# Kernel tuning notes

Hardware: AMD Instinct MI355X
Metric: run time of the kernel (lower is better)

Reference implementation:

```python
import jax, jax.numpy as jnp
import numpy as np

NIN = 128
NOUT = 128


def setup_inputs() -> dict:
    key = jax.random.key(0)
    k_adj, k_node, k_wi, k_wj = jax.random.split(key, 4)
    B, N = 4, 256
    adj = jax.random.uniform(k_adj, (B, 1, N, N), dtype=jnp.float32)
    node = jax.random.normal(k_node, (B, NIN, N), dtype=jnp.float32)
    # 1x1 conv weights, stored as [nout, nin] (squeezed from [nout, nin, 1, 1])
    scale = 1.0 / np.sqrt(NIN)
    Wi = jax.random.normal(k_wi, (NOUT, NIN), dtype=jnp.float32) * scale
    Wj = jax.random.normal(k_wj, (NOUT, NIN), dtype=jnp.float32) * scale
    return {"adj": adj, "node": node, "Wi": Wi, "Wj": Wj}


def reference(adj, node, Wi, Wj):
    # adj: [B,1,N,N], node: [B,nin,N]
    N = adj.shape[-1]
    # broadcast node across rows and mask by adjacency: [B,nin,N,N]
    x = node[:, :, None, :] * adj
    # 1x1 convs == channel contractions
    yi = jnp.einsum('oc,bcij->boij', Wi, x)
    yj = jnp.einsum('oc,bcij->boij', Wj, x)
    I = jnp.eye(N, dtype=x.dtype)
    return I * yi + (1.0 - I) * yj
```

## Files before the change

kernel.cpp:

```cpp
#include <hip/hip_runtime.h>

#define NIN  128
#define NOUT 128
#define NN   256
#define BB   4

__global__ __launch_bounds__(256) void nodeconv_kernel(
    const float* __restrict__ adj,
    const float* __restrict__ node,
    const float* __restrict__ Wi,
    const float* __restrict__ Wj,
    float* __restrict__ out)
{
    __shared__ float si[NN];
    __shared__ float sj[NN];

    const int bo = blockIdx.x;
    const int b  = bo >> 7;
    const int o  = bo & (NOUT - 1);
    const int t  = threadIdx.x;

    {
        const float* np_ = node + (size_t)(b * NIN) * NN + t;
        const float* wi  = Wi + o * NIN;
        const float* wj  = Wj + o * NIN;
        float ai = 0.f, aj = 0.f;
        #pragma unroll 8
        for (int c = 0; c < NIN; ++c) {
            const float n = np_[(size_t)c * NN];
            ai += wi[c] * n;
            aj += wj[c] * n;
        }
        si[t] = ai;
        sj[t] = aj;
    }
    __syncthreads();

    const int j4   = t & 63;
    const int jb   = j4 << 2;
    const int rrow = t >> 6;

    const float4 vj = *(const float4*)&sj[jb];

    const float* adjb = adj + (size_t)b * (NN * NN);
    float*       outp = out + (size_t)bo * (NN * NN);

    #pragma unroll 4
    for (int r = 0; r < 64; ++r) {
        const int i = (r << 2) + rrow;
        const float s_ii = si[i];
        const float4 a = *(const float4*)&adjb[i * NN + jb];
        float4 v;
        v.x = (i == jb + 0) ? s_ii : vj.x;
        v.y = (i == jb + 1) ? s_ii : vj.y;
        v.z = (i == jb + 2) ? s_ii : vj.z;
        v.w = (i == jb + 3) ? s_ii : vj.w;
        float4 rs;
        rs.x = a.x * v.x;
        rs.y = a.y * v.y;
        rs.z = a.z * v.z;
        rs.w = a.w * v.w;
        *(float4*)&outp[i * NN + jb] = rs;
    }
}

extern "C" void kernel_launch(void* const* d_in, const int* in_sizes, int n_in,
                              void* d_out, int out_size, void* d_ws, size_t ws_size,
                              hipStream_t stream) {
    const float* adj  = (const float*)d_in[0];
    const float* node = (const float*)d_in[1];
    const float* Wi   = (const float*)d_in[2];
    const float* Wj   = (const float*)d_in[3];
    float* out = (float*)d_out;

    dim3 grid(BB * NOUT);
    dim3 block(256);
    nodeconv_kernel<<<grid, block, 0, stream>>>(adj, node, Wi, Wj, out);
}
```

Before: 184.8 us.

## Split projection into precompute kernel and widen streaming grid eightfold

Moves the per-(batch,output) channel projection into its own kernel that writes ui/uj to workspace. A second kernel then streams adj times the projected values over a grid eight times larger, each block handling 32 rows. The aim is better occupancy and more latency hiding for the bandwidth-bound output write, since the old grid had only 512 blocks. The cost is an extra launch and a small workspace round trip. A fused fallback is kept for when the workspace is too small.

```diff
diff --git a/kernel.cpp b/kernel.cpp
--- a/kernel.cpp
+++ b/kernel.cpp
@@ -5,21 +5,83 @@
 #define NN   256
 #define BB   4
 
-__global__ __launch_bounds__(256) void nodeconv_kernel(
-    const float* __restrict__ adj,
+__global__ __launch_bounds__(256) void precompute_u(
     const float* __restrict__ node,
     const float* __restrict__ Wi,
     const float* __restrict__ Wj,
-    float* __restrict__ out)
+    float* __restrict__ ui,
+    float* __restrict__ uj)
 {
-    __shared__ float si[NN];
-    __shared__ float sj[NN];
-
     const int bo = blockIdx.x;
     const int b  = bo >> 7;
     const int o  = bo & (NOUT - 1);
     const int t  = threadIdx.x;
 
+    const float* np_ = node + (size_t)b * NIN * NN + t;
+    const float* wi  = Wi + o * NIN;
+    const float* wj  = Wj + o * NIN;
+
+    float ai = 0.f, aj = 0.f;
+    #pragma unroll 16
+    for (int c = 0; c < NIN; ++c) {
+        const float n = np_[c * NN];
+        ai = fmaf(wi[c], n, ai);
+        aj = fmaf(wj[c], n, aj);
+    }
+    ui[bo * NN + t] = ai;
+    uj[bo * NN + t] = aj;
+}
+
+__global__ __launch_bounds__(256) void stream_out(
+    const float* __restrict__ adj,
+    const float* __restrict__ ui,
+    const float* __restrict__ uj,
+    float* __restrict__ out)
+{
+    const int blk = blockIdx.x;
+    const int bo  = blk >> 3;
+    const int rc  = blk & 7;
+    const int b   = bo >> 7;
+    const int t   = threadIdx.x;
+    const int jb  = (t & 63) << 2;
+    const int rr  = t >> 6;
+
+    const float4 vj   = *(const float4*)&uj[bo * NN + jb];
+    const float* uip  = ui + bo * NN;
+    const float* adjb = adj + (size_t)b * (NN * NN);
+    float*       outp = out + (size_t)bo * (NN * NN);
+
+    const int i0 = (rc << 5) + rr;
+    #pragma unroll
+    for (int r = 0; r < 8; ++r) {
+        const int i = i0 + (r << 2);
+        const float s_ii = uip[i];
+        const float4 a = *(const float4*)&adjb[i * NN + jb];
+        float4 v;
+        v.x = (i == jb + 0) ? s_ii : vj.x;
+        v.y = (i == jb + 1) ? s_ii : vj.y;
+        v.z = (i == jb + 2) ? s_ii : vj.z;
+        v.w = (i == jb + 3) ? s_ii : vj.w;
+        float4 rs;
+        rs.x = a.x * v.x;
+        rs.y = a.y * v.y;
+        rs.z = a.z * v.z;
+        rs.w = a.w * v.w;
+        *(float4*)&outp[i * NN + jb] = rs;
+    }
+}
+
+__global__ __launch_bounds__(256) void nodeconv_fused(
+    const float* __restrict__ adj, const float* __restrict__ node,
+    const float* __restrict__ Wi, const float* __restrict__ Wj,
+    float* __restrict__ out)
+{
+    __shared__ float si[NN];
+    __shared__ float sj[NN];
+    const int bo = blockIdx.x;
+    const int b  = bo >> 7;
+    const int o  = bo & (NOUT - 1);
+    const int t  = threadIdx.x;
     {
         const float* np_ = node + (size_t)(b * NIN) * NN + t;
         const float* wi  = Wi + o * NIN;
@@ -35,16 +97,11 @@
         sj[t] = aj;
     }
     __syncthreads();
-
-    const int j4   = t & 63;
-    const int jb   = j4 << 2;
+    const int jb   = (t & 63) << 2;
     const int rrow = t >> 6;
-
     const float4 vj = *(const float4*)&sj[jb];
-
     const float* adjb = adj + (size_t)b * (NN * NN);
     float*       outp = out + (size_t)bo * (NN * NN);
-
     #pragma unroll 4
     for (int r = 0; r < 64; ++r) {
         const int i = (r << 2) + rrow;
@@ -56,10 +113,7 @@
         v.z = (i == jb + 2) ? s_ii : vj.z;
         v.w = (i == jb + 3) ? s_ii : vj.w;
         float4 rs;
-        rs.x = a.x * v.x;
-        rs.y = a.y * v.y;
-        rs.z = a.z * v.z;
-        rs.w = a.w * v.w;
+        rs.x = a.x * v.x; rs.y = a.y * v.y; rs.z = a.z * v.z; rs.w = a.w * v.w;
         *(float4*)&outp[i * NN + jb] = rs;
     }
 }
@@ -73,7 +127,15 @@
     const float* Wj   = (const float*)d_in[3];
     float* out = (float*)d_out;
 
-    dim3 grid(BB * NOUT);
-    dim3 block(256);
-    nodeconv_kernel<<<grid, block, 0, stream>>>(adj, node, Wi, Wj, out);
+    const size_t u_elems = (size_t)BB * NOUT * NN;
+    const size_t need    = 2 * u_elems * sizeof(float);
+
+    if (ws_size >= need) {
+        float* ui = (float*)d_ws;
+        float* uj = ui + u_elems;
+        precompute_u<<<dim3(BB * NOUT), dim3(256), 0, stream>>>(node, Wi, Wj, ui, uj);
+        stream_out<<<dim3(BB * NOUT * 8), dim3(256), 0, stream>>>(adj, ui, uj, out);
+    } else {
+        nodeconv_fused<<<dim3(BB * NOUT), dim3(256), 0, stream>>>(adj, node, Wi, Wj, out);
+    }
 }
```

Result: faster. 148.4 us (-19.7%).

## Use 1024-thread blocks with split-channel projection and nontemporal output stores

Applied to the files above, without the earlier changes.

Each block grows from 256 to 1024 threads. The per-node projection is split across four thread groups (two weight matrices times two halves of the channel dimension) and reduced through shared memory, which shortens the serial 128-step dot product. Each thread then writes 16 contiguous rows instead of 64 strided ones, using nontemporal stores for the large 128 MB output. Risks include an extra barrier and lower occupancy flexibility from the large block size.

```diff
diff --git a/kernel.cpp b/kernel.cpp
--- a/kernel.cpp
+++ b/kernel.cpp
@@ -5,13 +5,16 @@
 #define NN   256
 #define BB   4
 
-__global__ __launch_bounds__(256) void nodeconv_kernel(
+typedef float f4 __attribute__((ext_vector_type(4)));
+
+__global__ __launch_bounds__(1024, 2) void nodeconv_fused(
     const float* __restrict__ adj,
     const float* __restrict__ node,
     const float* __restrict__ Wi,
     const float* __restrict__ Wj,
     float* __restrict__ out)
 {
+    __shared__ float part[2][2][NN];
     __shared__ float si[NN];
     __shared__ float sj[NN];
 
@@ -21,46 +24,47 @@
     const int t  = threadIdx.x;
 
     {
-        const float* np_ = node + (size_t)(b * NIN) * NN + t;
-        const float* wi  = Wi + o * NIN;
-        const float* wj  = Wj + o * NIN;
-        float ai = 0.f, aj = 0.f;
-        #pragma unroll 8
-        for (int c = 0; c < NIN; ++c) {
-            const float n = np_[(size_t)c * NN];
-            ai += wi[c] * n;
-            aj += wj[c] * n;
-        }
-        si[t] = ai;
-        sj[t] = aj;
+        const int j   = t & 255;
+        const int sel = (t >> 8) & 1;
+        const int h   = t >> 9;
+        const float* w   = (sel ? Wj : Wi) + o * NIN + h * 64;
+        const float* np_ = node + ((size_t)b * NIN + h * 64) * NN + j;
+        float a = 0.f;
+        #pragma unroll 16
+        for (int c = 0; c < 64; ++c)
+            a = fmaf(w[c], np_[(size_t)c * NN], a);
+        part[h][sel][j] = a;
+    }
+    __syncthreads();
+    if (t < 512) {
+        const int j   = t & 255;
+        const int sel = t >> 8;
+        const float v = part[0][sel][j] + part[1][sel][j];
+        (sel ? sj : si)[j] = v;
     }
     __syncthreads();
 
-    const int j4   = t & 63;
-    const int jb   = j4 << 2;
-    const int rrow = t >> 6;
+    const int jb = (t & 63) << 2;
+    const int rr = t >> 6;
 
-    const float4 vj = *(const float4*)&sj[jb];
+    const f4 vj = *(const f4*)&sj[jb];
 
     const float* adjb = adj + (size_t)b * (NN * NN);
     float*       outp = out + (size_t)bo * (NN * NN);
 
-    #pragma unroll 4
-    for (int r = 0; r < 64; ++r) {
-        const int i = (r << 2) + rrow;
+    const int ibase = rr << 4;
+    #pragma unroll 8
+    for (int r = 0; r < 16; ++r) {
+        const int i = ibase + r;
         const float s_ii = si[i];
-        const float4 a = *(const float4*)&adjb[i * NN + jb];
-        float4 v;
+        const f4 a = *(const f4*)&adjb[i * NN + jb];
+        f4 v;
         v.x = (i == jb + 0) ? s_ii : vj.x;
         v.y = (i == jb + 1) ? s_ii : vj.y;
         v.z = (i == jb + 2) ? s_ii : vj.z;
         v.w = (i == jb + 3) ? s_ii : vj.w;
-        float4 rs;
-        rs.x = a.x * v.x;
-        rs.y = a.y * v.y;
-        rs.z = a.z * v.z;
-        rs.w = a.w * v.w;
-        *(float4*)&outp[i * NN + jb] = rs;
+        f4 rs = a * v;
+        __builtin_nontemporal_store(rs, (f4*)&outp[i * NN + jb]);
     }
 }
 
@@ -73,7 +77,5 @@
     const float* Wj   = (const float*)d_in[3];
     float* out = (float*)d_out;
 
-    dim3 grid(BB * NOUT);
-    dim3 block(256);
-    nodeconv_kernel<<<grid, block, 0, stream>>>(adj, node, Wi, Wj, out);
+    nodeconv_fused<<<dim3(BB * NOUT), dim3(1024), 0, stream>>>(adj, node, Wi, Wj, out);
 }
```

New measurement: 164.8 us. -10.8%, faster.
